# Kernel optimization log

Hardware: AMD Instinct MI355X
Metric: run time of the kernel (lower is better)

The kernel has to match this reference:

```python
import jax, jax.numpy as jnp
import numpy as np

H, W = 512, 512          # output image size (RenderLayer h, w)
CHUNK = 16               # faces per scan step in the rasterizer
BIG = 1e30
EPS = 1e-8


def _edge(ax, ay, bx, by, px, py):
    # 2D edge function (signed parallelogram area)
    return (px - ax) * (by - ay) - (py - ay) * (bx - ax)


def _project(v, campos, camrot, focal, princpt):
    # v: [N,V,3] -> camera space and pixel space (x_pix, y_pix, z_cam)
    v_cam = jnp.einsum('nij,nvj->nvi', camrot, v - campos[:, None])
    z = jnp.maximum(v_cam[..., 2:3], EPS)
    xy = jnp.einsum('nij,nvj->nvi', focal, v_cam[..., :2] / z) + princpt[:, None]
    v_pix = jnp.concatenate([xy, v_cam[..., 2:3]], axis=-1)
    return v_cam, v_pix


def _rasterize(v_pix, vi):
    # Z-buffer rasterization: returns per-pixel face index (-1 = background).
    N = v_pix.shape[0]
    F = vi.shape[0]
    px = jnp.arange(W, dtype=v_pix.dtype)[None, None, None, :]
    py = jnp.arange(H, dtype=v_pix.dtype)[None, None, :, None]
    tri = v_pix[:, vi]                       # [N,F,3,3]
    nchunks = F // CHUNK
    tri_c = jnp.moveaxis(tri.reshape(N, nchunks, CHUNK, 3, 3), 1, 0)  # [nc,N,C,3,3]
    base = jnp.arange(nchunks, dtype=jnp.int32) * CHUNK

    def body(carry, xs):
        best_d, best_i = carry
        t, b0 = xs                           # t: [N,C,3,3]
        x0 = t[:, :, 0, 0][..., None, None]; y0 = t[:, :, 0, 1][..., None, None]; z0 = t[:, :, 0, 2][..., None, None]
        x1 = t[:, :, 1, 0][..., None, None]; y1 = t[:, :, 1, 1][..., None, None]; z1 = t[:, :, 1, 2][..., None, None]
        x2 = t[:, :, 2, 0][..., None, None]; y2 = t[:, :, 2, 1][..., None, None]; z2 = t[:, :, 2, 2][..., None, None]
        w0 = _edge(x1, y1, x2, y2, px, py)   # [N,C,H,W]
        w1 = _edge(x2, y2, x0, y0, px, py)
        w2 = _edge(x0, y0, x1, y1, px, py)
        area = _edge(x0, y0, x1, y1, x2, y2)
        inside = (w0 * area >= 0) & (w1 * area >= 0) & (w2 * area >= 0) & (jnp.abs(area) > EPS)
        sa = jnp.where(jnp.abs(area) > EPS, area, 1.0)
        zi = (w0 / sa) / jnp.maximum(z0, EPS) + (w1 / sa) / jnp.maximum(z1, EPS) + (w2 / sa) / jnp.maximum(z2, EPS)
        valid = inside & (z0 > EPS) & (z1 > EPS) & (z2 > EPS) & (zi > EPS)
        d = jnp.where(valid, 1.0 / jnp.maximum(zi, EPS), BIG)
        d_min = jnp.min(d, axis=1)
        i_min = jnp.argmin(d, axis=1).astype(jnp.int32) + b0
        upd = d_min < best_d
        return (jnp.where(upd, d_min, best_d), jnp.where(upd, i_min, best_i)), None

    init = (jnp.full((N, H, W), BIG, v_pix.dtype), jnp.full((N, H, W), -1, jnp.int32))
    (best_d, best_i), _ = jax.lax.scan(body, init, (tri_c, base))
    mask = best_d < BIG
    return jnp.where(mask, best_i, -1), mask


def _interp(v_pix, vt, vi, vti, index_img, mask):
    # Perspective-correct barycentric interp of depth and texcoords (interp_vert_attrs)
    safe = jnp.maximum(index_img, 0)
    f_v = vi[safe]                            # [N,H,W,3]
    f_vt = vti[safe]
    pv = jax.vmap(lambda vp, t: vp[t])(v_pix, f_v)  # [N,H,W,3,3]
    px = jnp.arange(W, dtype=v_pix.dtype)[None, None, :]
    py = jnp.arange(H, dtype=v_pix.dtype)[None, :, None]
    x0, y0 = pv[..., 0, 0], pv[..., 0, 1]
    x1, y1 = pv[..., 1, 0], pv[..., 1, 1]
    x2, y2 = pv[..., 2, 0], pv[..., 2, 1]
    w0 = _edge(x1, y1, x2, y2, px, py)
    w1 = _edge(x2, y2, x0, y0, px, py)
    w2 = _edge(x0, y0, x1, y1, px, py)
    area = _edge(x0, y0, x1, y1, x2, y2)
    sa = jnp.where(jnp.abs(area) > EPS, area, 1.0)
    b = jnp.stack([w0, w1, w2], -1) / sa[..., None]     # screen-space bary [N,H,W,3]
    z = jnp.maximum(pv[..., 2], EPS)
    bz = b / z
    zi = jnp.maximum(jnp.sum(bz, -1, keepdims=True), EPS)
    bary = jnp.where(mask[..., None], bz / zi, 0.0)     # perspective-correct bary
    depth_img = jnp.where(mask, 1.0 / zi[..., 0], 0.0)
    vt_tri = vt[f_vt]                                   # [N,H,W,3,2]
    vt_img = jnp.einsum('nhwk,nhwkc->nhwc', bary, vt_tri)
    return depth_img, bary, vt_img


def _grid_sample_border(tex, grid):
    # torch.nn.functional.grid_sample: bilinear, padding_mode='border', align_corners=False
    N, C, Ht, Wt = tex.shape
    t = jnp.moveaxis(tex, 1, -1)              # [N,Ht,Wt,C]
    ix = (grid[..., 0] + 1.0) * 0.5 * Wt - 0.5
    iy = (grid[..., 1] + 1.0) * 0.5 * Ht - 0.5
    x0 = jnp.floor(ix); y0 = jnp.floor(iy)
    fx = (ix - x0)[..., None]; fy = (iy - y0)[..., None]
    x0i = jnp.clip(x0.astype(jnp.int32), 0, Wt - 1)
    x1i = jnp.clip(x0.astype(jnp.int32) + 1, 0, Wt - 1)
    y0i = jnp.clip(y0.astype(jnp.int32), 0, Ht - 1)
    y1i = jnp.clip(y0.astype(jnp.int32) + 1, 0, Ht - 1)
    gather = jax.vmap(lambda img, y, x: img[y, x])
    v00 = gather(t, y0i, x0i); v01 = gather(t, y0i, x1i)
    v10 = gather(t, y1i, x0i); v11 = gather(t, y1i, x1i)
    out = (v00 * (1 - fx) + v01 * fx) * (1 - fy) + (v10 * (1 - fx) + v11 * fx) * fy
    return jnp.moveaxis(out, -1, 1)           # [N,C,H,W]


def setup_inputs() -> dict:
    key = jax.random.key(0)
    ks = jax.random.split(key, 6)
    N, V, F, T = 2, 4096, 2048, 4096
    xy = jax.random.uniform(ks[0], (N, V, 2), minval=-1.0, maxval=1.0)
    z = jax.random.uniform(ks[1], (N, V, 1), minval=2.0, maxval=4.0)
    v = jnp.concatenate([xy, z], -1)
    tex = jax.random.normal(ks[2], (N, 3, 1024, 1024), dtype=jnp.float32)
    vt = jax.random.uniform(ks[3], (T, 2))
    vi = jax.random.randint(ks[4], (F, 3), 0, V, dtype=jnp.int32)
    vti = jax.random.randint(ks[5], (F, 3), 0, T, dtype=jnp.int32)
    campos = jnp.zeros((N, 3), jnp.float32)
    camrot = jnp.tile(jnp.eye(3, dtype=jnp.float32)[None], (N, 1, 1))
    focal = jnp.tile(jnp.array([[512.0, 0.0], [0.0, 512.0]], jnp.float32)[None], (N, 1, 1))
    princpt = jnp.full((N, 2), 256.0, jnp.float32)
    return {"v": v, "tex": tex, "vt": vt, "vi": vi, "vti": vti,
            "campos": campos, "camrot": camrot, "focal": focal, "princpt": princpt}


def reference(v, tex, vt, vi, vti, campos, camrot, focal, princpt):
    vt = vt.at[:, 1].set(1.0 - vt[:, 1])      # flip_uvs=True buffer transform
    v_cam, v_pix = _project(v, campos, camrot, focal, princpt)
    index_img, mask = _rasterize(jax.lax.stop_gradient(v_pix), vi)
    depth_img, bary, vt_img = _interp(v_pix, vt, vi, vti, index_img, mask)
    grid = vt_img * 2.0 - 1.0                 # uv in [0,1] -> grid_sample coords
    render = _grid_sample_border(tex, grid) * mask[:, None].astype(tex.dtype)
    bary_img = jnp.moveaxis(bary, -1, 1)
    return render, mask.astype(jnp.float32), depth_img, vt_img, bary_img, index_img
```

## Files before the change

### kernel.cpp

```cpp
#include <hip/hip_runtime.h>
#include <math.h>

#define EPSD 1e-8
#define EPSF 1e-8f
#define IMG_H 512
#define IMG_W 512
#define TEX_W 1024
#define TEX_H 1024
#define REJ_SLACK 1e-3
#define FULL_THR 16.0

__global__ __launch_bounds__(256) void k_project(
    const float* __restrict__ v,
    const float* __restrict__ campos,
    const float* __restrict__ camrot,
    const float* __restrict__ focal,
    const float* __restrict__ princpt,
    double* __restrict__ vpixd,
    int N, int V) {
#pragma clang fp contract(off)
  int i = blockIdx.x * blockDim.x + threadIdx.x;
  if (i >= N * V) return;
  int n = i / V;
  const float* vv = v + (size_t)i * 3;
  double ax = (double)vv[0] - (double)campos[n * 3 + 0];
  double ay = (double)vv[1] - (double)campos[n * 3 + 1];
  double az = (double)vv[2] - (double)campos[n * 3 + 2];
  const float* R = camrot + (size_t)n * 9;
  double cx = ((double)R[0] * ax + (double)R[1] * ay) + (double)R[2] * az;
  double cy = ((double)R[3] * ax + (double)R[4] * ay) + (double)R[5] * az;
  double cz = ((double)R[6] * ax + (double)R[7] * ay) + (double)R[8] * az;
  double zz = fmax(cz, EPSD);
  double xd = cx / zz;
  double yd = cy / zz;
  const float* Fc = focal + (size_t)n * 4;
  double px = ((double)Fc[0] * xd + (double)Fc[1] * yd) + (double)princpt[n * 2 + 0];
  double py = ((double)Fc[2] * xd + (double)Fc[3] * yd) + (double)princpt[n * 2 + 1];
  vpixd[(size_t)i * 3 + 0] = px;
  vpixd[(size_t)i * 3 + 1] = py;
  vpixd[(size_t)i * 3 + 2] = cz;
}

__global__ __launch_bounds__(256) void k_setup(
    const double* __restrict__ vpixd,
    const int* __restrict__ vi,
    double2* __restrict__ tri,
    float4* __restrict__ bbox,
    int N, int V, int F) {
#pragma clang fp contract(off)
  int i = blockIdx.x * blockDim.x + threadIdx.x;
  if (i >= N * F) return;
  int n = i / F;
  int f = i - n * F;
  int i0 = vi[f * 3 + 0], i1 = vi[f * 3 + 1], i2 = vi[f * 3 + 2];
  const double* p0 = vpixd + ((size_t)n * V + i0) * 3;
  const double* p1 = vpixd + ((size_t)n * V + i1) * 3;
  const double* p2 = vpixd + ((size_t)n * V + i2) * 3;
  double x0 = p0[0], y0 = p0[1], z0 = p0[2];
  double x1 = p1[0], y1 = p1[1], z1 = p1[2];
  double x2 = p2[0], y2 = p2[1], z2 = p2[2];
  double A0 = y2 - y1, B0 = x2 - x1;
  double A1 = y0 - y2, B1 = x0 - x2;
  double A2 = y1 - y0, B2 = x1 - x0;
  double area = (x2 - x0) * A2 - (y2 - y0) * B2;
  bool valid = (fabs(area) > EPSD) && (z0 > EPSD) && (z1 > EPSD) && (z2 > EPSD);
  double s = area;
  double EA0 = 0.0, EB0 = 0.0, EC0 = -1.0;
  double EA1 = 0.0, EB1 = 0.0, EC1 = -1.0;
  double EA2 = 0.0, EB2 = 0.0, EC2 = -1.0;
  double P = 0.0, Q = 0.0, S = 0.0;
  if (valid) {
    EA0 = A0 * s; EB0 = -(B0 * s); EC0 = (y1 * B0 - x1 * A0) * s;
    EA1 = A1 * s; EB1 = -(B1 * s); EC1 = (y2 * B1 - x2 * A1) * s;
    EA2 = A2 * s; EB2 = -(B2 * s); EC2 = (y0 * B2 - x0 * A2) * s;
    double s2 = s * s;
    double R0 = 1.0 / (s2 * fmax(z0, EPSD));
    double R1 = 1.0 / (s2 * fmax(z1, EPSD));
    double R2 = 1.0 / (s2 * fmax(z2, EPSD));
    P = EA0 * R0 + EA1 * R1 + EA2 * R2;
    S = EB0 * R0 + EB1 * R1 + EB2 * R2;
    Q = EC0 * R0 + EC1 * R1 + EC2 * R2;
  }
  double2* T = tri + (size_t)i * 6;
  T[0] = make_double2(EA0, EB0);
  T[1] = make_double2(EC0, EA1);
  T[2] = make_double2(EB1, EC1);
  T[3] = make_double2(EA2, EB2);
  T[4] = make_double2(EC2, P);
  T[5] = make_double2(Q, S);
  float mnx = (float)fmin(x0, fmin(x1, x2));
  float mny = (float)fmin(y0, fmin(y1, y2));
  float mxx = (float)fmax(x0, fmax(x1, x2));
  float mxy = (float)fmax(y0, fmax(y1, y2));
  bbox[i] = make_float4(mnx, mny, mxx, mxy);
}

__global__ __launch_bounds__(256, 2) void k_raster(
    const double2* __restrict__ tri,
    const float4* __restrict__ bbox,
    float* __restrict__ out_idx,
    int F) {
  __shared__ __align__(16) char smem[25600];
  double2* s_tri = (double2*)smem;
  int* s_idx = (int*)(smem + 24576);
  double* zbuf = (double*)smem;
  int* ibuf = (int*)(smem + 8192);

  int n = blockIdx.z;
  int tid = threadIdx.x;
  int w = tid >> 6, lane = tid & 63;
  int xl = lane & 15, yb = (lane >> 4) * 4;
  int x = blockIdx.x * 16 + xl;
  int ytop = blockIdx.y * 16;
  double px = (double)x;
  double py0 = (double)(ytop + yb);
  float tminx = (float)(blockIdx.x * 16) - 0.5f;
  float tmaxx = tminx + 16.0f;
  float tminy = (float)ytop - 0.5f;
  float tmaxy = tminy + 16.0f;
  double X0 = (double)(blockIdx.x * 16), X1 = X0 + 15.0;
  double Y0 = (double)ytop, Y1 = Y0 + 15.0;

  double bz[4];
  int bi[4];
#pragma unroll
  for (int r = 0; r < 4; ++r) { bz[r] = EPSD; bi[r] = -1; }

  const double2* trin = tri + (size_t)n * F * 6;
  const float4* bbn = bbox + (size_t)n * F;
  int FQ = (F + 3) >> 2;
  int fbeg = w * FQ;
  int fend = min(F, fbeg + FQ);
  int NR = (fend > fbeg) ? ((fend - fbeg + 63) >> 6) : 0;
  double2* s_tri_w = s_tri + (size_t)w * (64 * 6);
  int* s_idx_w = s_idx + w * 64;
  unsigned long long lmask = (1ull << lane) - 1ull;

  int cnt = 0;
  auto survLoop = [&]() {
    int last = cnt - 1;
    double2 c0 = s_tri_w[0], c1 = s_tri_w[1], c2 = s_tri_w[2],
            c3 = s_tri_w[3], c4 = s_tri_w[4], c5 = s_tri_w[5];
    int enc = s_idx_w[0];
    for (int u = 0; u < cnt; ++u) {
      int un = min(u + 1, last);
      const double2* Tn = s_tri_w + (size_t)un * 6;
      double2 m0 = Tn[0], m1 = Tn[1], m2 = Tn[2];
      double2 m3 = Tn[3], m4 = Tn[4], m5 = Tn[5];
      int en = s_idx_w[un];
      int e = __builtin_amdgcn_readfirstlane(enc);
      int ti = e & 0x7fffffff;
      double uu = fma(px, c4.y, c5.x);
      double py = py0;
      if (e < 0) {
#pragma unroll
        for (int r = 0; r < 4; ++r) {
          double zi = fma(py, c5.y, uu);
          if (zi > bz[r]) { bz[r] = zi; bi[r] = ti; }
          py += 1.0;
        }
      } else {
        double q0 = fma(px, c0.x, c1.x);
        double q1 = fma(px, c1.y, c2.y);
        double q2 = fma(px, c3.x, c4.x);
#pragma unroll
        for (int r = 0; r < 4; ++r) {
          double W0 = fma(py, c0.y, q0);
          double W1 = fma(py, c2.x, q1);
          double W2 = fma(py, c3.y, q2);
          double zi = fma(py, c5.y, uu);
          int msk = (__double2hiint(W0) | __double2hiint(W1) |
                     __double2hiint(W2)) >> 31;
          zi = __hiloint2double(__double2hiint(zi) | msk, __double2loint(zi));
          if (zi > bz[r]) { bz[r] = zi; bi[r] = ti; }
          py += 1.0;
        }
      }
      c0 = m0; c1 = m1; c2 = m2; c3 = m3; c4 = m4; c5 = m5; enc = en;
    }
  };

  float4 bbB = make_float4(0.f, 0.f, 0.f, 0.f);
  bool bbpA = false;
  double2 A0, A1, A2, A3, A4, A5;
  if (NR > 0) {
    int t0 = fbeg + lane;
    float4 bbA;
    if (t0 < fend) bbA = bbn[t0];
    bbpA = (t0 < fend) &&
           !(bbA.z < tminx || bbA.x > tmaxx || bbA.w < tminy || bbA.y > tmaxy);
    if (bbpA) {
      const double2* T = trin + (size_t)t0 * 6;
      A0 = T[0]; A1 = T[1]; A2 = T[2]; A3 = T[3]; A4 = T[4]; A5 = T[5];
    }
    if (t0 + 64 < fend) bbB = bbn[t0 + 64];
  }
  for (int r = 0; r < NR; ++r) {
    int t = fbeg + (r << 6) + lane;
    if (cnt > 0) survLoop();
    asm volatile("s_waitcnt lgkmcnt(0)" ::: "memory");
    bool surv = false, full = false;
    if (bbpA) {
      double xs0 = (A0.x >= 0.0) ? X1 : X0;
      double ys0 = (A0.y >= 0.0) ? Y1 : Y0;
      double w0M = fma(ys0, A0.y, fma(xs0, A0.x, A1.x));
      double xs1 = (A1.y >= 0.0) ? X1 : X0;
      double ys1 = (A2.x >= 0.0) ? Y1 : Y0;
      double w1M = fma(ys1, A2.x, fma(xs1, A1.y, A2.y));
      double xs2 = (A3.x >= 0.0) ? X1 : X0;
      double ys2 = (A3.y >= 0.0) ? Y1 : Y0;
      double w2M = fma(ys2, A3.y, fma(xs2, A3.x, A4.x));
      surv = (w0M >= -REJ_SLACK) & (w1M >= -REJ_SLACK) & (w2M >= -REJ_SLACK);
      if (surv) {
        double xn0 = (A0.x >= 0.0) ? X0 : X1;
        double yn0 = (A0.y >= 0.0) ? Y0 : Y1;
        double w0m = fma(yn0, A0.y, fma(xn0, A0.x, A1.x));
        double xn1 = (A1.y >= 0.0) ? X0 : X1;
        double yn1 = (A2.x >= 0.0) ? Y0 : Y1;
        double w1m = fma(yn1, A2.x, fma(xn1, A1.y, A2.y));
        double xn2 = (A3.x >= 0.0) ? X0 : X1;
        double yn2 = (A3.y >= 0.0) ? Y0 : Y1;
        double w2m = fma(yn2, A3.y, fma(xn2, A3.x, A4.x));
        full = (w0m >= FULL_THR) & (w1m >= FULL_THR) & (w2m >= FULL_THR);
      }
    }
    unsigned long long m = __ballot(surv);
    cnt = (int)__popcll(m);
    if (surv) {
      int dst = (int)__popcll(m & lmask);
      double2* d = s_tri_w + (size_t)dst * 6;
      d[0] = A0; d[1] = A1; d[2] = A2; d[3] = A3; d[4] = A4; d[5] = A5;
      s_idx_w[dst] = t | (full ? (int)0x80000000 : 0);
    }
    asm volatile("s_waitcnt lgkmcnt(0)" ::: "memory");
    int tn1 = t + 64;
    bool bbpB = (tn1 < fend) &&
                !(bbB.z < tminx || bbB.x > tmaxx || bbB.w < tminy || bbB.y > tmaxy);
    if (bbpB) {
      const double2* T = trin + (size_t)tn1 * 6;
      A0 = T[0]; A1 = T[1]; A2 = T[2]; A3 = T[3]; A4 = T[4]; A5 = T[5];
    }
    if (tn1 + 64 < fend) bbB = bbn[tn1 + 64];
    bbpA = bbpB;
  }
  if (cnt > 0) survLoop();

  __syncthreads();
#pragma unroll
  for (int r = 0; r < 4; ++r) {
    int pix = (yb + r) * 16 + xl;
    zbuf[w * 256 + pix] = bz[r];
    ibuf[w * 256 + pix] = bi[r];
  }
  __syncthreads();
  {
    int pix = tid;
    double z = zbuf[pix];
    int i = ibuf[pix];
#pragma unroll
    for (int q = 1; q < 4; ++q) {
      double zq = zbuf[q * 256 + pix];
      int iq = ibuf[q * 256 + pix];
      bool take = (zq > z) || ((zq == z) && ((unsigned)iq < (unsigned)i));
      if (take) { z = zq; i = iq; }
    }
    int yloc = pix >> 4, xloc = pix & 15;
    size_t g = (size_t)n * IMG_H * IMG_W +
               (size_t)(ytop + yloc) * IMG_W + (blockIdx.x * 16 + xloc);
    out_idx[g] = (float)i;
  }
}

__global__ __launch_bounds__(256) void k_interp(
    const double* __restrict__ vpixd,
    const float* __restrict__ vt,
    const int* __restrict__ vi,
    const int* __restrict__ vti,
    const float* __restrict__ tex,
    float* __restrict__ out,
    int N, int V) {
#pragma clang fp contract(off)
  const int HW = IMG_H * IMG_W;
  int gid = blockIdx.x * blockDim.x + threadIdx.x;
  if (gid >= N * HW) return;
  int n = gid / HW;
  int p = gid - n * HW;
  int y = p / IMG_W;
  int x = p - y * IMG_W;
  size_t NHW = (size_t)N * HW;
  float* out_render = out;
  float* out_mask = out + 3 * NHW;
  float* out_depth = out + 4 * NHW;
  float* out_vt = out + 5 * NHW;
  float* out_bary = out + 7 * NHW;
  float* out_idx = out + 10 * NHW;

  int idx = (int)out_idx[gid];
  if (idx < 0) {
    for (int c = 0; c < 3; ++c) out_render[(size_t)(n * 3 + c) * HW + p] = 0.0f;
    out_mask[gid] = 0.0f;
    out_depth[gid] = 0.0f;
    out_vt[(size_t)gid * 2 + 0] = 0.0f;
    out_vt[(size_t)gid * 2 + 1] = 0.0f;
    for (int k = 0; k < 3; ++k) out_bary[(size_t)(n * 3 + k) * HW + p] = 0.0f;
    return;
  }
  int f0 = vi[idx * 3 + 0], f1 = vi[idx * 3 + 1], f2 = vi[idx * 3 + 2];
  int t0i = vti[idx * 3 + 0], t1i = vti[idx * 3 + 1], t2i = vti[idx * 3 + 2];
  const double* pv0 = vpixd + ((size_t)n * V + f0) * 3;
  const double* pv1 = vpixd + ((size_t)n * V + f1) * 3;
  const double* pv2 = vpixd + ((size_t)n * V + f2) * 3;
  float x0 = (float)pv0[0], y0 = (float)pv0[1], z0 = (float)pv0[2];
  float x1 = (float)pv1[0], y1 = (float)pv1[1], z1 = (float)pv1[2];
  float x2 = (float)pv2[0], y2 = (float)pv2[1], z2 = (float)pv2[2];
  float px = (float)x, py = (float)y;
  float w0 = (px - x1) * (y2 - y1) - (py - y1) * (x2 - x1);
  float w1 = (px - x2) * (y0 - y2) - (py - y2) * (x0 - x2);
  float w2 = (px - x0) * (y1 - y0) - (py - y0) * (x1 - x0);
  float area = (x2 - x0) * (y1 - y0) - (y2 - y0) * (x1 - x0);
  float sa = (fabsf(area) > EPSF) ? area : 1.0f;
  float b0 = w0 / sa, b1 = w1 / sa, b2 = w2 / sa;
  float zz0 = fmaxf(z0, EPSF), zz1 = fmaxf(z1, EPSF), zz2 = fmaxf(z2, EPSF);
  float bz0 = b0 / zz0, bz1 = b1 / zz1, bz2 = b2 / zz2;
  float zi = fmaxf((bz0 + bz1) + bz2, EPSF);
  float r0 = bz0 / zi, r1 = bz1 / zi, r2 = bz2 / zi;
  float depth = 1.0f / zi;
  float u0 = vt[(size_t)t0i * 2 + 0], q0 = 1.0f - vt[(size_t)t0i * 2 + 1];
  float u1 = vt[(size_t)t1i * 2 + 0], q1 = 1.0f - vt[(size_t)t1i * 2 + 1];
  float u2 = vt[(size_t)t2i * 2 + 0], q2 = 1.0f - vt[(size_t)t2i * 2 + 1];
  float vtx = (r0 * u0 + r1 * u1) + r2 * u2;
  float vty = (r0 * q0 + r1 * q1) + r2 * q2;
  float gx = vtx * 2.0f - 1.0f;
  float gy = vty * 2.0f - 1.0f;
  float ix = ((gx + 1.0f) * 0.5f) * (float)TEX_W - 0.5f;
  float iy = ((gy + 1.0f) * 0.5f) * (float)TEX_H - 0.5f;
  float x0f = floorf(ix), y0f = floorf(iy);
  float fx = ix - x0f, fy = iy - y0f;
  int x0i = min(max((int)x0f, 0), TEX_W - 1);
  int x1i = min(max((int)x0f + 1, 0), TEX_W - 1);
  int y0i = min(max((int)y0f, 0), TEX_H - 1);
  int y1i = min(max((int)y0f + 1, 0), TEX_H - 1);
  float omfx = 1.0f - fx, omfy = 1.0f - fy;
  for (int c = 0; c < 3; ++c) {
    const float* tc = tex + (size_t)(n * 3 + c) * TEX_H * TEX_W;
    float v00 = tc[(size_t)y0i * TEX_W + x0i];
    float v01 = tc[(size_t)y0i * TEX_W + x1i];
    float v10 = tc[(size_t)y1i * TEX_W + x0i];
    float v11 = tc[(size_t)y1i * TEX_W + x1i];
    float o = (v00 * omfx + v01 * fx) * omfy + (v10 * omfx + v11 * fx) * fy;
    out_render[(size_t)(n * 3 + c) * HW + p] = o;
  }
  out_mask[gid] = 1.0f;
  out_depth[gid] = depth;
  out_vt[(size_t)gid * 2 + 0] = vtx;
  out_vt[(size_t)gid * 2 + 1] = vty;
  out_bary[(size_t)(n * 3 + 0) * HW + p] = r0;
  out_bary[(size_t)(n * 3 + 1) * HW + p] = r1;
  out_bary[(size_t)(n * 3 + 2) * HW + p] = r2;
}

extern "C" void kernel_launch(void* const* d_in, const int* in_sizes, int n_in,
                              void* d_out, int out_size, void* d_ws, size_t ws_size,
                              hipStream_t stream) {
  const float* v = (const float*)d_in[0];
  const float* tex = (const float*)d_in[1];
  const float* vt = (const float*)d_in[2];
  const int* vi = (const int*)d_in[3];
  const int* vti = (const int*)d_in[4];
  const float* campos = (const float*)d_in[5];
  const float* camrot = (const float*)d_in[6];
  const float* focal = (const float*)d_in[7];
  const float* princpt = (const float*)d_in[8];
  int N = in_sizes[5] / 3;
  int V = in_sizes[0] / (3 * N);
  int F = in_sizes[3] / 3;

  char* wp = (char*)d_ws;
  double* vpixd = (double*)wp;
  wp += sizeof(double) * (size_t)N * V * 3;
  double2* tri = (double2*)wp;
  wp += sizeof(double2) * (size_t)N * F * 6;
  float4* bbox = (float4*)wp;

  const int HW = IMG_H * IMG_W;
  const size_t NHW = (size_t)N * HW;
  float* out_idx = (float*)d_out + (size_t)10 * NHW;

  int nv = N * V;
  k_project<<<(nv + 255) / 256, 256, 0, stream>>>(v, campos, camrot, focal,
                                                  princpt, vpixd, N, V);
  int nf = N * F;
  k_setup<<<(nf + 255) / 256, 256, 0, stream>>>(vpixd, vi, tri, bbox, N, V, F);
  dim3 rgrid(IMG_W / 16, IMG_H / 16, N);
  k_raster<<<rgrid, dim3(256, 1, 1), 0, stream>>>(tri, bbox, out_idx, F);
  int np = N * HW;
  k_interp<<<(np + 255) / 256, 256, 0, stream>>>(vpixd, vt, vi, vti, tex,
                                                 (float*)d_out, N, V);
}
```

Before: 201.9 us.

## Use persistent raster blocks with atomic tile stealing in center-out spiral order

The rasterizer now launches a fixed pool of persistent blocks that fetch tiles from a global atomic counter instead of one block per tile. Tiles are handed out in a spiral from the image center outward, so the likely heavy central tiles start first and the light border tiles fill in the tail. The counter is reset in the setup kernel. This is meant to reduce load imbalance across tiles with very different triangle counts, at the cost of an atomic and an extra barrier per tile.

Measured after the change: 183.0 us. -9.4%, faster.

```diff
diff --git a/kernel.cpp b/kernel.cpp
--- a/kernel.cpp
+++ b/kernel.cpp
@@ -9,6 +9,9 @@
 #define TEX_H 1024
 #define REJ_SLACK 1e-3
 #define FULL_THR 16.0
+#define TILES_X (IMG_W / 16)
+#define TILES_Y (IMG_H / 16)
+#define TILES_PER_IMG (TILES_X * TILES_Y)
 
 __global__ __launch_bounds__(256) void k_project(
     const float* __restrict__ v,
@@ -46,9 +49,11 @@
     const int* __restrict__ vi,
     double2* __restrict__ tri,
     float4* __restrict__ bbox,
+    int* __restrict__ counter,
     int N, int V, int F) {
 #pragma clang fp contract(off)
   int i = blockIdx.x * blockDim.x + threadIdx.x;
+  if (i == 0) counter[0] = 0;
   if (i >= N * F) return;
   int n = i / F;
   int f = i - n * F;
@@ -95,179 +100,208 @@
   bbox[i] = make_float4(mnx, mny, mxx, mxy);
 }
 
+__device__ inline void steal_to_tile(int s, int& tx, int& ty) {
+  int k = (int)(__fsqrt_rn((float)s) * 0.5f);
+  while (k > 0 && 4 * k * k > s) --k;
+  while (4 * (k + 1) * (k + 1) <= s) ++k;
+  int o = s - 4 * k * k;
+  int L = 2 * k + 2;
+  int x0 = TILES_X / 2 - 1 - k, y0 = TILES_Y / 2 - 1 - k;
+  int side = o / (L - 1);
+  int off = o - side * (L - 1);
+  if (side == 0)      { tx = x0 + off;         ty = y0; }
+  else if (side == 1) { tx = x0 + L - 1;       ty = y0 + off; }
+  else if (side == 2) { tx = x0 + L - 1 - off; ty = y0 + L - 1; }
+  else                { tx = x0;               ty = y0 + L - 1 - off; }
+}
+
 __global__ __launch_bounds__(256, 2) void k_raster(
     const double2* __restrict__ tri,
     const float4* __restrict__ bbox,
+    int* __restrict__ counter,
     float* __restrict__ out_idx,
-    int F) {
+    int N, int F) {
   __shared__ __align__(16) char smem[25600];
   double2* s_tri = (double2*)smem;
   int* s_idx = (int*)(smem + 24576);
   double* zbuf = (double*)smem;
   int* ibuf = (int*)(smem + 8192);
-
-  int n = blockIdx.z;
+  __shared__ int s_steal;
+
   int tid = threadIdx.x;
   int w = tid >> 6, lane = tid & 63;
   int xl = lane & 15, yb = (lane >> 4) * 4;
-  int x = blockIdx.x * 16 + xl;
-  int ytop = blockIdx.y * 16;
-  double px = (double)x;
-  double py0 = (double)(ytop + yb);
-  float tminx = (float)(blockIdx.x * 16) - 0.5f;
-  float tmaxx = tminx + 16.0f;
-  float tminy = (float)ytop - 0.5f;
-  float tmaxy = tminy + 16.0f;
-  double X0 = (double)(blockIdx.x * 16), X1 = X0 + 15.0;
-  double Y0 = (double)ytop, Y1 = Y0 + 15.0;
-
-  double bz[4];
-  int bi[4];
-#pragma unroll
-  for (int r = 0; r < 4; ++r) { bz[r] = EPSD; bi[r] = -1; }
-
-  const double2* trin = tri + (size_t)n * F * 6;
-  const float4* bbn = bbox + (size_t)n * F;
+  unsigned long long lmask = (1ull << lane) - 1ull;
   int FQ = (F + 3) >> 2;
   int fbeg = w * FQ;
   int fend = min(F, fbeg + FQ);
   int NR = (fend > fbeg) ? ((fend - fbeg + 63) >> 6) : 0;
   double2* s_tri_w = s_tri + (size_t)w * (64 * 6);
   int* s_idx_w = s_idx + w * 64;
-  unsigned long long lmask = (1ull << lane) - 1ull;
-
-  int cnt = 0;
-  auto survLoop = [&]() {
-    int last = cnt - 1;
-    double2 c0 = s_tri_w[0], c1 = s_tri_w[1], c2 = s_tri_w[2],
-            c3 = s_tri_w[3], c4 = s_tri_w[4], c5 = s_tri_w[5];
-    int enc = s_idx_w[0];
-    for (int u = 0; u < cnt; ++u) {
-      int un = min(u + 1, last);
-      const double2* Tn = s_tri_w + (size_t)un * 6;
-      double2 m0 = Tn[0], m1 = Tn[1], m2 = Tn[2];
-      double2 m3 = Tn[3], m4 = Tn[4], m5 = Tn[5];
-      int en = s_idx_w[un];
-      int e = __builtin_amdgcn_readfirstlane(enc);
-      int ti = e & 0x7fffffff;
-      double uu = fma(px, c4.y, c5.x);
-      double py = py0;
-      if (e < 0) {
+  const int TOT = N * TILES_PER_IMG;
+
+  for (;;) {
+    if (tid == 0) s_steal = atomicAdd(counter, 1);
+    __syncthreads();
+    int s = s_steal;
+    if (s >= TOT) break;
+    int n = s % N;
+    int q = s / N;
+    int tx, ty;
+    steal_to_tile(q, tx, ty);
+
+    int x = tx * 16 + xl;
+    int ytop = ty * 16;
+    double px = (double)x;
+    double py0 = (double)(ytop + yb);
+    float tminx = (float)(tx * 16) - 0.5f;
+    float tmaxx = tminx + 16.0f;
+    float tminy = (float)ytop - 0.5f;
+    float tmaxy = tminy + 16.0f;
+    double X0 = (double)(tx * 16), X1 = X0 + 15.0;
+    double Y0 = (double)ytop, Y1 = Y0 + 15.0;
+
+    double bz[4];
+    int bi[4];
 #pragma unroll
-        for (int r = 0; r < 4; ++r) {
-          double zi = fma(py, c5.y, uu);
-          if (zi > bz[r]) { bz[r] = zi; bi[r] = ti; }
-          py += 1.0;
+    for (int r = 0; r < 4; ++r) { bz[r] = EPSD; bi[r] = -1; }
+
+    const double2* trin = tri + (size_t)n * F * 6;
+    const float4* bbn = bbox + (size_t)n * F;
+
+    int cnt = 0;
+    auto survLoop = [&]() {
+      int last = cnt - 1;
+      double2 c0 = s_tri_w[0], c1 = s_tri_w[1], c2 = s_tri_w[2],
+              c3 = s_tri_w[3], c4 = s_tri_w[4], c5 = s_tri_w[5];
+      int enc = s_idx_w[0];
+      for (int u = 0; u < cnt; ++u) {
+        int un = min(u + 1, last);
+        const double2* Tn = s_tri_w + (size_t)un * 6;
+        double2 m0 = Tn[0], m1 = Tn[1], m2 = Tn[2];
+        double2 m3 = Tn[3], m4 = Tn[4], m5 = Tn[5];
+        int en = s_idx_w[un];
+        int e = __builtin_amdgcn_readfirstlane(enc);
+        int ti = e & 0x7fffffff;
+        double uu = fma(px, c4.y, c5.x);
+        double py = py0;
+        if (e < 0) {
+#pragma unroll
+          for (int r = 0; r < 4; ++r) {
+            double zi = fma(py, c5.y, uu);
+            if (zi > bz[r]) { bz[r] = zi; bi[r] = ti; }
+            py += 1.0;
+          }
+        } else {
+          double q0 = fma(px, c0.x, c1.x);
+          double q1 = fma(px, c1.y, c2.y);
+          double q2 = fma(px, c3.x, c4.x);
+#pragma unroll
+          for (int r = 0; r < 4; ++r) {
+            double W0 = fma(py, c0.y, q0);
+            double W1 = fma(py, c2.x, q1);
+            double W2 = fma(py, c3.y, q2);
+            double zi = fma(py, c5.y, uu);
+            int msk = (__double2hiint(W0) | __double2hiint(W1) |
+                       __double2hiint(W2)) >> 31;
+            zi = __hiloint2double(__double2hiint(zi) | msk, __double2loint(zi));
+            if (zi > bz[r]) { bz[r] = zi; bi[r] = ti; }
+            py += 1.0;
+          }
         }
-      } else {
-        double q0 = fma(px, c0.x, c1.x);
-        double q1 = fma(px, c1.y, c2.y);
-        double q2 = fma(px, c3.x, c4.x);
+        c0 = m0; c1 = m1; c2 = m2; c3 = m3; c4 = m4; c5 = m5; enc = en;
+      }
+    };
+
+    float4 bbB = make_float4(0.f, 0.f, 0.f, 0.f);
+    bool bbpA = false;
+    double2 A0, A1, A2, A3, A4, A5;
+    if (NR > 0) {
+      int t0 = fbeg + lane;
+      float4 bbA;
+      if (t0 < fend) bbA = bbn[t0];
+      bbpA = (t0 < fend) &&
+             !(bbA.z < tminx || bbA.x > tmaxx || bbA.w < tminy || bbA.y > tmaxy);
+      if (bbpA) {
+        const double2* T = trin + (size_t)t0 * 6;
+        A0 = T[0]; A1 = T[1]; A2 = T[2]; A3 = T[3]; A4 = T[4]; A5 = T[5];
+      }
+      if (t0 + 64 < fend) bbB = bbn[t0 + 64];
+    }
+    for (int r = 0; r < NR; ++r) {
+      int t = fbeg + (r << 6) + lane;
+      if (cnt > 0) survLoop();
+      asm volatile("s_waitcnt lgkmcnt(0)" ::: "memory");
+      bool surv = false, full = false;
+      if (bbpA) {
+        double xs0 = (A0.x >= 0.0) ? X1 : X0;
+        double ys0 = (A0.y >= 0.0) ? Y1 : Y0;
+        double w0M = fma(ys0, A0.y, fma(xs0, A0.x, A1.x));
+        double xs1 = (A1.y >= 0.0) ? X1 : X0;
+        double ys1 = (A2.x >= 0.0) ? Y1 : Y0;
+        double w1M = fma(ys1, A2.x, fma(xs1, A1.y, A2.y));
+        double xs2 = (A3.x >= 0.0) ? X1 : X0;
+        double ys2 = (A3.y >= 0.0) ? Y1 : Y0;
+        double w2M = fma(ys2, A3.y, fma(xs2, A3.x, A4.x));
+        surv = (w0M >= -REJ_SLACK) & (w1M >= -REJ_SLACK) & (w2M >= -REJ_SLACK);
+        if (surv) {
+          double xn0 = (A0.x >= 0.0) ? X0 : X1;
+          double yn0 = (A0.y >= 0.0) ? Y0 : Y1;
+          double w0m = fma(yn0, A0.y, fma(xn0, A0.x, A1.x));
+          double xn1 = (A1.y >= 0.0) ? X0 : X1;
+          double yn1 = (A2.x >= 0.0) ? Y0 : Y1;
+          double w1m = fma(yn1, A2.x, fma(xn1, A1.y, A2.y));
+          double xn2 = (A3.x >= 0.0) ? X0 : X1;
+          double yn2 = (A3.y >= 0.0) ? Y0 : Y1;
+          double w2m = fma(yn2, A3.y, fma(xn2, A3.x, A4.x));
+          full = (w0m >= FULL_THR) & (w1m >= FULL_THR) & (w2m >= FULL_THR);
+        }
+      }
+      unsigned long long m = __ballot(surv);
+      cnt = (int)__popcll(m);
+      if (surv) {
+        int dst = (int)__popcll(m & lmask);
+        double2* d = s_tri_w + (size_t)dst * 6;
+        d[0] = A0; d[1] = A1; d[2] = A2; d[3] = A3; d[4] = A4; d[5] = A5;
+        s_idx_w[dst] = t | (full ? (int)0x80000000 : 0);
+      }
+      asm volatile("s_waitcnt lgkmcnt(0)" ::: "memory");
+      int tn1 = t + 64;
+      bool bbpB = (tn1 < fend) &&
+                  !(bbB.z < tminx || bbB.x > tmaxx || bbB.w < tminy || bbB.y > tmaxy);
+      if (bbpB) {
+        const double2* T = trin + (size_t)tn1 * 6;
+        A0 = T[0]; A1 = T[1]; A2 = T[2]; A3 = T[3]; A4 = T[4]; A5 = T[5];
+      }
+      if (tn1 + 64 < fend) bbB = bbn[tn1 + 64];
+      bbpA = bbpB;
+    }
+    if (cnt > 0) survLoop();
+
+    __syncthreads();
 #pragma unroll
-        for (int r = 0; r < 4; ++r) {
-          double W0 = fma(py, c0.y, q0);
-          double W1 = fma(py, c2.x, q1);
-          double W2 = fma(py, c3.y, q2);
-          double zi = fma(py, c5.y, uu);
-          int msk = (__double2hiint(W0) | __double2hiint(W1) |
-                     __double2hiint(W2)) >> 31;
-          zi = __hiloint2double(__double2hiint(zi) | msk, __double2loint(zi));
-          if (zi > bz[r]) { bz[r] = zi; bi[r] = ti; }
-          py += 1.0;
-        }
-      }
-      c0 = m0; c1 = m1; c2 = m2; c3 = m3; c4 = m4; c5 = m5; enc = en;
+    for (int r = 0; r < 4; ++r) {
+      int pix = (yb + r) * 16 + xl;
+      zbuf[w * 256 + pix] = bz[r];
+      ibuf[w * 256 + pix] = bi[r];
     }
-  };
-
-  float4 bbB = make_float4(0.f, 0.f, 0.f, 0.f);
-  bool bbpA = false;
-  double2 A0, A1, A2, A3, A4, A5;
-  if (NR > 0) {
-    int t0 = fbeg + lane;
-    float4 bbA;
-    if (t0 < fend) bbA = bbn[t0];
-    bbpA = (t0 < fend) &&
-           !(bbA.z < tminx || bbA.x > tmaxx || bbA.w < tminy || bbA.y > tmaxy);
-    if (bbpA) {
-      const double2* T = trin + (size_t)t0 * 6;
-      A0 = T[0]; A1 = T[1]; A2 = T[2]; A3 = T[3]; A4 = T[4]; A5 = T[5];
+    __syncthreads();
+    {
+      int pix = tid;
+      double z = zbuf[pix];
+      int i = ibuf[pix];
+#pragma unroll
+      for (int qq = 1; qq < 4; ++qq) {
+        double zq = zbuf[qq * 256 + pix];
+        int iq = ibuf[qq * 256 + pix];
+        bool take = (zq > z) || ((zq == z) && ((unsigned)iq < (unsigned)i));
+        if (take) { z = zq; i = iq; }
+      }
+      int yloc = pix >> 4, xloc = pix & 15;
+      size_t g = (size_t)n * IMG_H * IMG_W +
+                 (size_t)(ytop + yloc) * IMG_W + (tx * 16 + xloc);
+      out_idx[g] = (float)i;
     }
-    if (t0 + 64 < fend) bbB = bbn[t0 + 64];
-  }
-  for (int r = 0; r < NR; ++r) {
-    int t = fbeg + (r << 6) + lane;
-    if (cnt > 0) survLoop();
-    asm volatile("s_waitcnt lgkmcnt(0)" ::: "memory");
-    bool surv = false, full = false;
-    if (bbpA) {
-      double xs0 = (A0.x >= 0.0) ? X1 : X0;
-      double ys0 = (A0.y >= 0.0) ? Y1 : Y0;
-      double w0M = fma(ys0, A0.y, fma(xs0, A0.x, A1.x));
-      double xs1 = (A1.y >= 0.0) ? X1 : X0;
-      double ys1 = (A2.x >= 0.0) ? Y1 : Y0;
-      double w1M = fma(ys1, A2.x, fma(xs1, A1.y, A2.y));
-      double xs2 = (A3.x >= 0.0) ? X1 : X0;
-      double ys2 = (A3.y >= 0.0) ? Y1 : Y0;
-      double w2M = fma(ys2, A3.y, fma(xs2, A3.x, A4.x));
-      surv = (w0M >= -REJ_SLACK) & (w1M >= -REJ_SLACK) & (w2M >= -REJ_SLACK);
-      if (surv) {
-        double xn0 = (A0.x >= 0.0) ? X0 : X1;
-        double yn0 = (A0.y >= 0.0) ? Y0 : Y1;
-        double w0m = fma(yn0, A0.y, fma(xn0, A0.x, A1.x));
-        double xn1 = (A1.y >= 0.0) ? X0 : X1;
-        double yn1 = (A2.x >= 0.0) ? Y0 : Y1;
-        double w1m = fma(yn1, A2.x, fma(xn1, A1.y, A2.y));
-        double xn2 = (A3.x >= 0.0) ? X0 : X1;
-        double yn2 = (A3.y >= 0.0) ? Y0 : Y1;
-        double w2m = fma(yn2, A3.y, fma(xn2, A3.x, A4.x));
-        full = (w0m >= FULL_THR) & (w1m >= FULL_THR) & (w2m >= FULL_THR);
-      }
-    }
-    unsigned long long m = __ballot(surv);
-    cnt = (int)__popcll(m);
-    if (surv) {
-      int dst = (int)__popcll(m & lmask);
-      double2* d = s_tri_w + (size_t)dst * 6;
-      d[0] = A0; d[1] = A1; d[2] = A2; d[3] = A3; d[4] = A4; d[5] = A5;
-      s_idx_w[dst] = t | (full ? (int)0x80000000 : 0);
-    }
-    asm volatile("s_waitcnt lgkmcnt(0)" ::: "memory");
-    int tn1 = t + 64;
-    bool bbpB = (tn1 < fend) &&
-                !(bbB.z < tminx || bbB.x > tmaxx || bbB.w < tminy || bbB.y > tmaxy);
-    if (bbpB) {
-      const double2* T = trin + (size_t)tn1 * 6;
-      A0 = T[0]; A1 = T[1]; A2 = T[2]; A3 = T[3]; A4 = T[4]; A5 = T[5];
-    }
-    if (tn1 + 64 < fend) bbB = bbn[tn1 + 64];
-    bbpA = bbpB;
-  }
-  if (cnt > 0) survLoop();
-
-  __syncthreads();
-#pragma unroll
-  for (int r = 0; r < 4; ++r) {
-    int pix = (yb + r) * 16 + xl;
-    zbuf[w * 256 + pix] = bz[r];
-    ibuf[w * 256 + pix] = bi[r];
-  }
-  __syncthreads();
-  {
-    int pix = tid;
-    double z = zbuf[pix];
-    int i = ibuf[pix];
-#pragma unroll
-    for (int q = 1; q < 4; ++q) {
-      double zq = zbuf[q * 256 + pix];
-      int iq = ibuf[q * 256 + pix];
-      bool take = (zq > z) || ((zq == z) && ((unsigned)iq < (unsigned)i));
-      if (take) { z = zq; i = iq; }
-    }
-    int yloc = pix >> 4, xloc = pix & 15;
-    size_t g = (size_t)n * IMG_H * IMG_W +
-               (size_t)(ytop + yloc) * IMG_W + (blockIdx.x * 16 + xloc);
-    out_idx[g] = (float)i;
   }
 }
 
@@ -381,6 +415,8 @@
   double2* tri = (double2*)wp;
   wp += sizeof(double2) * (size_t)N * F * 6;
   float4* bbox = (float4*)wp;
+  wp += sizeof(float4) * (size_t)N * F;
+  int* counter = (int*)wp;
 
   const int HW = IMG_H * IMG_W;
   const size_t NHW = (size_t)N * HW;
@@ -390,9 +426,12 @@
   k_project<<<(nv + 255) / 256, 256, 0, stream>>>(v, campos, camrot, focal,
                                                   princpt, vpixd, N, V);
   int nf = N * F;
-  k_setup<<<(nf + 255) / 256, 256, 0, stream>>>(vpixd, vi, tri, bbox, N, V, F);
-  dim3 rgrid(IMG_W / 16, IMG_H / 16, N);
-  k_raster<<<rgrid, dim3(256, 1, 1), 0, stream>>>(tri, bbox, out_idx, F);
+  k_setup<<<(nf + 255) / 256, 256, 0, stream>>>(vpixd, vi, tri, bbox, counter,
+                                                N, V, F);
+  int nblk = 1536;
+  int tot = N * TILES_PER_IMG;
+  if (nblk > tot) nblk = tot;
+  k_raster<<<nblk, 256, 0, stream>>>(tri, bbox, counter, out_idx, N, F);
   int np = N * HW;
   k_interp<<<(np + 255) / 256, 256, 0, stream>>>(vpixd, vt, vi, vti, tex,
                                                  (float*)d_out, N, V);
```

## Fuse interpolation into rasterizer and assign one 16x8 tile per wavefront

Applied to the files above, without the earlier changes.

Each wavefront now owns its own 16x8 pixel tile and scans all faces, replacing the old scheme where four waves split the face list of a 16x16 tile and merged z-buffers through shared memory. The interpolation and texture-sampling stage is fused into the raster kernel, so the per-pixel face index goes straight from registers into the output instead of a write and reload through global memory, and one kernel launch is removed. In exchange each wave culls the full face list alone and does divergent per-pixel gather work at the end. The tie-break on equal depth now depends only on face scan order within the wave.

Measured after the change: 248.1 us. 1.23x slower.

```diff
diff --git a/kernel.cpp b/kernel.cpp
--- a/kernel.cpp
+++ b/kernel.cpp
@@ -9,6 +9,11 @@
 #define TEX_H 1024
 #define REJ_SLACK 1e-3
 #define FULL_THR 16.0
+#define TILE_W 16
+#define TILE_H 8
+#define TILES_X (IMG_W / TILE_W)
+#define TILES_Y (IMG_H / TILE_H)
+#define TILES_PER_IMG (TILES_X * TILES_Y)
 
 __global__ __launch_bounds__(256) void k_project(
     const float* __restrict__ v,
@@ -98,40 +103,48 @@
 __global__ __launch_bounds__(256, 2) void k_raster(
     const double2* __restrict__ tri,
     const float4* __restrict__ bbox,
-    float* __restrict__ out_idx,
-    int F) {
+    const double* __restrict__ vpixd,
+    const float* __restrict__ vt,
+    const int* __restrict__ vi,
+    const int* __restrict__ vti,
+    const float* __restrict__ tex,
+    float* __restrict__ out,
+    int N, int V, int F) {
+#pragma clang fp contract(off)
   __shared__ __align__(16) char smem[25600];
   double2* s_tri = (double2*)smem;
   int* s_idx = (int*)(smem + 24576);
-  double* zbuf = (double*)smem;
-  int* ibuf = (int*)(smem + 8192);
-
-  int n = blockIdx.z;
+
   int tid = threadIdx.x;
   int w = tid >> 6, lane = tid & 63;
-  int xl = lane & 15, yb = (lane >> 4) * 4;
-  int x = blockIdx.x * 16 + xl;
-  int ytop = blockIdx.y * 16;
+  int g = blockIdx.x * 4 + w;
+  const int TOT = N * TILES_PER_IMG;
+  if (g >= TOT) return;
+  int n = g / TILES_PER_IMG;
+  int q = g - n * TILES_PER_IMG;
+  int tx = q & (TILES_X - 1);
+  int ty = q >> 5;
+
+  int xl = lane & 15, yb = (lane >> 4) * 2;
+  int x = tx * TILE_W + xl;
+  int ytop = ty * TILE_H;
   double px = (double)x;
   double py0 = (double)(ytop + yb);
-  float tminx = (float)(blockIdx.x * 16) - 0.5f;
-  float tmaxx = tminx + 16.0f;
+  float tminx = (float)(tx * TILE_W) - 0.5f;
+  float tmaxx = tminx + (float)TILE_W;
   float tminy = (float)ytop - 0.5f;
-  float tmaxy = tminy + 16.0f;
-  double X0 = (double)(blockIdx.x * 16), X1 = X0 + 15.0;
-  double Y0 = (double)ytop, Y1 = Y0 + 15.0;
-
-  double bz[4];
-  int bi[4];
+  float tmaxy = tminy + (float)TILE_H;
+  double X0 = (double)(tx * TILE_W), X1 = X0 + (double)(TILE_W - 1);
+  double Y0 = (double)ytop, Y1 = Y0 + (double)(TILE_H - 1);
+
+  double bz[2];
+  int bi[2];
 #pragma unroll
-  for (int r = 0; r < 4; ++r) { bz[r] = EPSD; bi[r] = -1; }
+  for (int r = 0; r < 2; ++r) { bz[r] = EPSD; bi[r] = -1; }
 
   const double2* trin = tri + (size_t)n * F * 6;
   const float4* bbn = bbox + (size_t)n * F;
-  int FQ = (F + 3) >> 2;
-  int fbeg = w * FQ;
-  int fend = min(F, fbeg + FQ);
-  int NR = (fend > fbeg) ? ((fend - fbeg + 63) >> 6) : 0;
+  int NR = (F + 63) >> 6;
   double2* s_tri_w = s_tri + (size_t)w * (64 * 6);
   int* s_idx_w = s_idx + w * 64;
   unsigned long long lmask = (1ull << lane) - 1ull;
@@ -154,7 +167,7 @@
       double py = py0;
       if (e < 0) {
 #pragma unroll
-        for (int r = 0; r < 4; ++r) {
+        for (int r = 0; r < 2; ++r) {
           double zi = fma(py, c5.y, uu);
           if (zi > bz[r]) { bz[r] = zi; bi[r] = ti; }
           py += 1.0;
@@ -164,7 +177,7 @@
         double q1 = fma(px, c1.y, c2.y);
         double q2 = fma(px, c3.x, c4.x);
 #pragma unroll
-        for (int r = 0; r < 4; ++r) {
+        for (int r = 0; r < 2; ++r) {
           double W0 = fma(py, c0.y, q0);
           double W1 = fma(py, c2.x, q1);
           double W2 = fma(py, c3.y, q2);
@@ -183,20 +196,20 @@
   float4 bbB = make_float4(0.f, 0.f, 0.f, 0.f);
   bool bbpA = false;
   double2 A0, A1, A2, A3, A4, A5;
-  if (NR > 0) {
-    int t0 = fbeg + lane;
+  {
+    int t0 = lane;
     float4 bbA;
-    if (t0 < fend) bbA = bbn[t0];
-    bbpA = (t0 < fend) &&
+    if (t0 < F) bbA = bbn[t0];
+    bbpA = (t0 < F) &&
            !(bbA.z < tminx || bbA.x > tmaxx || bbA.w < tminy || bbA.y > tmaxy);
     if (bbpA) {
       const double2* T = trin + (size_t)t0 * 6;
       A0 = T[0]; A1 = T[1]; A2 = T[2]; A3 = T[3]; A4 = T[4]; A5 = T[5];
     }
-    if (t0 + 64 < fend) bbB = bbn[t0 + 64];
+    if (t0 + 64 < F) bbB = bbn[t0 + 64];
   }
   for (int r = 0; r < NR; ++r) {
-    int t = fbeg + (r << 6) + lane;
+    int t = (r << 6) + lane;
     if (cnt > 0) survLoop();
     asm volatile("s_waitcnt lgkmcnt(0)" ::: "memory");
     bool surv = false, full = false;
@@ -234,60 +247,19 @@
     }
     asm volatile("s_waitcnt lgkmcnt(0)" ::: "memory");
     int tn1 = t + 64;
-    bool bbpB = (tn1 < fend) &&
+    bool bbpB = (tn1 < F) &&
                 !(bbB.z < tminx || bbB.x > tmaxx || bbB.w < tminy || bbB.y > tmaxy);
     if (bbpB) {
       const double2* T = trin + (size_t)tn1 * 6;
       A0 = T[0]; A1 = T[1]; A2 = T[2]; A3 = T[3]; A4 = T[4]; A5 = T[5];
     }
-    if (tn1 + 64 < fend) bbB = bbn[tn1 + 64];
+    if (tn1 + 64 < F) bbB = bbn[tn1 + 64];
     bbpA = bbpB;
   }
   if (cnt > 0) survLoop();
 
-  __syncthreads();
-#pragma unroll
-  for (int r = 0; r < 4; ++r) {
-    int pix = (yb + r) * 16 + xl;
-    zbuf[w * 256 + pix] = bz[r];
-    ibuf[w * 256 + pix] = bi[r];
-  }
-  __syncthreads();
-  {
-    int pix = tid;
-    double z = zbuf[pix];
-    int i = ibuf[pix];
-#pragma unroll
-    for (int q = 1; q < 4; ++q) {
-      double zq = zbuf[q * 256 + pix];
-      int iq = ibuf[q * 256 + pix];
-      bool take = (zq > z) || ((zq == z) && ((unsigned)iq < (unsigned)i));
-      if (take) { z = zq; i = iq; }
-    }
-    int yloc = pix >> 4, xloc = pix & 15;
-    size_t g = (size_t)n * IMG_H * IMG_W +
-               (size_t)(ytop + yloc) * IMG_W + (blockIdx.x * 16 + xloc);
-    out_idx[g] = (float)i;
-  }
-}
-
-__global__ __launch_bounds__(256) void k_interp(
-    const double* __restrict__ vpixd,
-    const float* __restrict__ vt,
-    const int* __restrict__ vi,
-    const int* __restrict__ vti,
-    const float* __restrict__ tex,
-    float* __restrict__ out,
-    int N, int V) {
-#pragma clang fp contract(off)
   const int HW = IMG_H * IMG_W;
-  int gid = blockIdx.x * blockDim.x + threadIdx.x;
-  if (gid >= N * HW) return;
-  int n = gid / HW;
-  int p = gid - n * HW;
-  int y = p / IMG_W;
-  int x = p - y * IMG_W;
-  size_t NHW = (size_t)N * HW;
+  const size_t NHW = (size_t)N * HW;
   float* out_render = out;
   float* out_mask = out + 3 * NHW;
   float* out_depth = out + 4 * NHW;
@@ -295,68 +267,75 @@
   float* out_bary = out + 7 * NHW;
   float* out_idx = out + 10 * NHW;
 
-  int idx = (int)out_idx[gid];
-  if (idx < 0) {
-    for (int c = 0; c < 3; ++c) out_render[(size_t)(n * 3 + c) * HW + p] = 0.0f;
-    out_mask[gid] = 0.0f;
-    out_depth[gid] = 0.0f;
-    out_vt[(size_t)gid * 2 + 0] = 0.0f;
-    out_vt[(size_t)gid * 2 + 1] = 0.0f;
-    for (int k = 0; k < 3; ++k) out_bary[(size_t)(n * 3 + k) * HW + p] = 0.0f;
-    return;
+#pragma unroll
+  for (int r = 0; r < 2; ++r) {
+    int y = ytop + yb + r;
+    int p = y * IMG_W + x;
+    size_t gid = (size_t)n * HW + p;
+    int idx = bi[r];
+    out_idx[gid] = (float)idx;
+    if (idx < 0) {
+      for (int c = 0; c < 3; ++c) out_render[(size_t)(n * 3 + c) * HW + p] = 0.0f;
+      out_mask[gid] = 0.0f;
+      out_depth[gid] = 0.0f;
+      out_vt[(size_t)gid * 2 + 0] = 0.0f;
+      out_vt[(size_t)gid * 2 + 1] = 0.0f;
+      for (int k = 0; k < 3; ++k) out_bary[(size_t)(n * 3 + k) * HW + p] = 0.0f;
+    } else {
+      int f0 = vi[idx * 3 + 0], f1 = vi[idx * 3 + 1], f2 = vi[idx * 3 + 2];
+      int t0i = vti[idx * 3 + 0], t1i = vti[idx * 3 + 1], t2i = vti[idx * 3 + 2];
+      const double* pv0 = vpixd + ((size_t)n * V + f0) * 3;
+      const double* pv1 = vpixd + ((size_t)n * V + f1) * 3;
+      const double* pv2 = vpixd + ((size_t)n * V + f2) * 3;
+      float x0 = (float)pv0[0], y0 = (float)pv0[1], z0 = (float)pv0[2];
+      float x1 = (float)pv1[0], y1 = (float)pv1[1], z1 = (float)pv1[2];
+      float x2 = (float)pv2[0], y2 = (float)pv2[1], z2 = (float)pv2[2];
+      float pxf = (float)x, pyf = (float)y;
+      float w0 = (pxf - x1) * (y2 - y1) - (pyf - y1) * (x2 - x1);
+      float w1 = (pxf - x2) * (y0 - y2) - (pyf - y2) * (x0 - x2);
+      float w2 = (pxf - x0) * (y1 - y0) - (pyf - y0) * (x1 - x0);
+      float area = (x2 - x0) * (y1 - y0) - (y2 - y0) * (x1 - x0);
+      float sa = (fabsf(area) > EPSF) ? area : 1.0f;
+      float b0 = w0 / sa, b1 = w1 / sa, b2 = w2 / sa;
+      float zz0 = fmaxf(z0, EPSF), zz1 = fmaxf(z1, EPSF), zz2 = fmaxf(z2, EPSF);
+      float bz0 = b0 / zz0, bz1 = b1 / zz1, bz2 = b2 / zz2;
+      float zi = fmaxf((bz0 + bz1) + bz2, EPSF);
+      float r0 = bz0 / zi, r1 = bz1 / zi, r2 = bz2 / zi;
+      float depth = 1.0f / zi;
+      float u0 = vt[(size_t)t0i * 2 + 0], q0 = 1.0f - vt[(size_t)t0i * 2 + 1];
+      float u1 = vt[(size_t)t1i * 2 + 0], q1 = 1.0f - vt[(size_t)t1i * 2 + 1];
+      float u2 = vt[(size_t)t2i * 2 + 0], q2 = 1.0f - vt[(size_t)t2i * 2 + 1];
+      float vtx = (r0 * u0 + r1 * u1) + r2 * u2;
+      float vty = (r0 * q0 + r1 * q1) + r2 * q2;
+      float gx = vtx * 2.0f - 1.0f;
+      float gy = vty * 2.0f - 1.0f;
+      float ix = ((gx + 1.0f) * 0.5f) * (float)TEX_W - 0.5f;
+      float iy = ((gy + 1.0f) * 0.5f) * (float)TEX_H - 0.5f;
+      float x0f = floorf(ix), y0f = floorf(iy);
+      float fx = ix - x0f, fy = iy - y0f;
+      int x0i = min(max((int)x0f, 0), TEX_W - 1);
+      int x1i = min(max((int)x0f + 1, 0), TEX_W - 1);
+      int y0i = min(max((int)y0f, 0), TEX_H - 1);
+      int y1i = min(max((int)y0f + 1, 0), TEX_H - 1);
+      float omfx = 1.0f - fx, omfy = 1.0f - fy;
+      for (int c = 0; c < 3; ++c) {
+        const float* tc = tex + (size_t)(n * 3 + c) * TEX_H * TEX_W;
+        float v00 = tc[(size_t)y0i * TEX_W + x0i];
+        float v01 = tc[(size_t)y0i * TEX_W + x1i];
+        float v10 = tc[(size_t)y1i * TEX_W + x0i];
+        float v11 = tc[(size_t)y1i * TEX_W + x1i];
+        float o = (v00 * omfx + v01 * fx) * omfy + (v10 * omfx + v11 * fx) * fy;
+        out_render[(size_t)(n * 3 + c) * HW + p] = o;
+      }
+      out_mask[gid] = 1.0f;
+      out_depth[gid] = depth;
+      out_vt[(size_t)gid * 2 + 0] = vtx;
+      out_vt[(size_t)gid * 2 + 1] = vty;
+      out_bary[(size_t)(n * 3 + 0) * HW + p] = r0;
+      out_bary[(size_t)(n * 3 + 1) * HW + p] = r1;
+      out_bary[(size_t)(n * 3 + 2) * HW + p] = r2;
+    }
   }
-  int f0 = vi[idx * 3 + 0], f1 = vi[idx * 3 + 1], f2 = vi[idx * 3 + 2];
-  int t0i = vti[idx * 3 + 0], t1i = vti[idx * 3 + 1], t2i = vti[idx * 3 + 2];
-  const double* pv0 = vpixd + ((size_t)n * V + f0) * 3;
-  const double* pv1 = vpixd + ((size_t)n * V + f1) * 3;
-  const double* pv2 = vpixd + ((size_t)n * V + f2) * 3;
-  float x0 = (float)pv0[0], y0 = (float)pv0[1], z0 = (float)pv0[2];
-  float x1 = (float)pv1[0], y1 = (float)pv1[1], z1 = (float)pv1[2];
-  float x2 = (float)pv2[0], y2 = (float)pv2[1], z2 = (float)pv2[2];
-  float px = (float)x, py = (float)y;
-  float w0 = (px - x1) * (y2 - y1) - (py - y1) * (x2 - x1);
-  float w1 = (px - x2) * (y0 - y2) - (py - y2) * (x0 - x2);
-  float w2 = (px - x0) * (y1 - y0) - (py - y0) * (x1 - x0);
-  float area = (x2 - x0) * (y1 - y0) - (y2 - y0) * (x1 - x0);
-  float sa = (fabsf(area) > EPSF) ? area : 1.0f;
-  float b0 = w0 / sa, b1 = w1 / sa, b2 = w2 / sa;
-  float zz0 = fmaxf(z0, EPSF), zz1 = fmaxf(z1, EPSF), zz2 = fmaxf(z2, EPSF);
-  float bz0 = b0 / zz0, bz1 = b1 / zz1, bz2 = b2 / zz2;
-  float zi = fmaxf((bz0 + bz1) + bz2, EPSF);
-  float r0 = bz0 / zi, r1 = bz1 / zi, r2 = bz2 / zi;
-  float depth = 1.0f / zi;
-  float u0 = vt[(size_t)t0i * 2 + 0], q0 = 1.0f - vt[(size_t)t0i * 2 + 1];
-  float u1 = vt[(size_t)t1i * 2 + 0], q1 = 1.0f - vt[(size_t)t1i * 2 + 1];
-  float u2 = vt[(size_t)t2i * 2 + 0], q2 = 1.0f - vt[(size_t)t2i * 2 + 1];
-  float vtx = (r0 * u0 + r1 * u1) + r2 * u2;
-  float vty = (r0 * q0 + r1 * q1) + r2 * q2;
-  float gx = vtx * 2.0f - 1.0f;
-  float gy = vty * 2.0f - 1.0f;
-  float ix = ((gx + 1.0f) * 0.5f) * (float)TEX_W - 0.5f;
-  float iy = ((gy + 1.0f) * 0.5f) * (float)TEX_H - 0.5f;
-  float x0f = floorf(ix), y0f = floorf(iy);
-  float fx = ix - x0f, fy = iy - y0f;
-  int x0i = min(max((int)x0f, 0), TEX_W - 1);
-  int x1i = min(max((int)x0f + 1, 0), TEX_W - 1);
-  int y0i = min(max((int)y0f, 0), TEX_H - 1);
-  int y1i = min(max((int)y0f + 1, 0), TEX_H - 1);
-  float omfx = 1.0f - fx, omfy = 1.0f - fy;
-  for (int c = 0; c < 3; ++c) {
-    const float* tc = tex + (size_t)(n * 3 + c) * TEX_H * TEX_W;
-    float v00 = tc[(size_t)y0i * TEX_W + x0i];
-    float v01 = tc[(size_t)y0i * TEX_W + x1i];
-    float v10 = tc[(size_t)y1i * TEX_W + x0i];
-    float v11 = tc[(size_t)y1i * TEX_W + x1i];
-    float o = (v00 * omfx + v01 * fx) * omfy + (v10 * omfx + v11 * fx) * fy;
-    out_render[(size_t)(n * 3 + c) * HW + p] = o;
-  }
-  out_mask[gid] = 1.0f;
-  out_depth[gid] = depth;
-  out_vt[(size_t)gid * 2 + 0] = vtx;
-  out_vt[(size_t)gid * 2 + 1] = vty;
-  out_bary[(size_t)(n * 3 + 0) * HW + p] = r0;
-  out_bary[(size_t)(n * 3 + 1) * HW + p] = r1;
-  out_bary[(size_t)(n * 3 + 2) * HW + p] = r2;
 }
 
 extern "C" void kernel_launch(void* const* d_in, const int* in_sizes, int n_in,
@@ -382,18 +361,13 @@
   wp += sizeof(double2) * (size_t)N * F * 6;
   float4* bbox = (float4*)wp;
 
-  const int HW = IMG_H * IMG_W;
-  const size_t NHW = (size_t)N * HW;
-  float* out_idx = (float*)d_out + (size_t)10 * NHW;
-
   int nv = N * V;
   k_project<<<(nv + 255) / 256, 256, 0, stream>>>(v, campos, camrot, focal,
                                                   princpt, vpixd, N, V);
   int nf = N * F;
   k_setup<<<(nf + 255) / 256, 256, 0, stream>>>(vpixd, vi, tri, bbox, N, V, F);
-  dim3 rgrid(IMG_W / 16, IMG_H / 16, N);
-  k_raster<<<rgrid, dim3(256, 1, 1), 0, stream>>>(tri, bbox, out_idx, F);
-  int np = N * HW;
-  k_interp<<<(np + 255) / 256, 256, 0, stream>>>(vpixd, vt, vi, vti, tex,
-                                                 (float*)d_out, N, V);
+  int tot = N * TILES_PER_IMG;
+  int nblk = (tot + 3) / 4;
+  k_raster<<<nblk, 256, 0, stream>>>(tri, bbox, vpixd, vt, vi, vti, tex,
+                                     (float*)d_out, N, V, F);
 }
```
